# Performance work log

Measured on AMD Instinct MI355X. Metric: run time of the kernel, lower is better.

## Reference

```python
import jax, jax.numpy as jnp
import numpy as np

B, S, D, H = 4, 2048, 1024, 16
DK = D // H


def setup_inputs() -> dict:
    key = jax.random.key(0)
    kx, kq, kk, kv, ko = jax.random.split(key, 5)
    scale = D ** -0.5
    return {
        "x": jax.random.normal(kx, (B, S, D), dtype=jnp.float32),
        "W_q": jax.random.normal(kq, (D, D), dtype=jnp.float32) * scale,
        "W_k": jax.random.normal(kk, (D, D), dtype=jnp.float32) * scale,
        "W_v": jax.random.normal(kv, (D, D), dtype=jnp.float32) * scale,
        "W_o": jax.random.normal(ko, (D, D), dtype=jnp.float32) * scale,
    }


def reference(x, W_q, W_k, W_v, W_o):
    b, s, d = x.shape
    # projections: x @ W.T  (weights stored [out, in])
    def proj(W):
        return (x @ W.T).reshape(b, s, H, DK).transpose(0, 2, 1, 3)  # [b,h,s,dk]
    Q, K, V = proj(W_q), proj(W_k), proj(W_v)
    scores = jnp.einsum('bhqd,bhkd->bhqk', Q, K) * (DK ** -0.5)
    causal = jnp.tril(jnp.ones((s, s), dtype=bool))
    scores = jnp.where(causal, scores, -jnp.inf)
    attn = jax.nn.softmax(scores, axis=-1)
    out = jnp.einsum('bhqk,bhkd->bhqd', attn, V)  # [b,h,s,dk]
    out = out.transpose(0, 2, 1, 3).reshape(b, s, d)
    return out @ W_o.T
```

## Files before the change

kernel.cpp:

```cpp
#include <hip/hip_runtime.h>
#include <stdint.h>

#define B_ 4
#define S_ 2048
#define D_ 1024
#define H_ 16
#define DK_ 64
#define M_ (B_*S_)

typedef __attribute__((ext_vector_type(8))) short bhalf8;
typedef __attribute__((ext_vector_type(4))) short bhalf4;
typedef __attribute__((ext_vector_type(4))) float floatx4;
typedef unsigned short bfu;
typedef unsigned int u32;

__device__ __forceinline__ bfu f2bf(float f) {
  union { float f; u32 u; } v; v.f = f;
  u32 r = v.u + 0x7FFFu + ((v.u >> 16) & 1u);
  return (bfu)(r >> 16);
}

__device__ __forceinline__ u32 cvtpk(float a, float b) {
  u32 r;
  asm("v_cvt_pk_bf16_f32 %0, %1, %2" : "=v"(r) : "v"(a), "v"(b));
  return r;
}

__device__ __forceinline__ void gll16(const bfu* g, bfu* l) {
  __builtin_amdgcn_global_load_lds((__attribute__((address_space(1))) void*)g,
                                   (__attribute__((address_space(3))) void*)l,
                                   16, 0, 0);
}

__global__ void cvt_all(const float* __restrict__ x,  const float* __restrict__ wq,
                        const float* __restrict__ wk, const float* __restrict__ wv,
                        const float* __restrict__ wo, bfu* __restrict__ dst) {
  const size_t u = ((size_t)blockIdx.x * blockDim.x + threadIdx.x) * 4;
  const size_t XN = (size_t)M_ * D_;
  const float* src;
  if (u < XN) {
    src = x + u;
  } else {
    const size_t v = u - XN;
    const int wsel = (int)(v >> 20);
    const size_t off = v & ((size_t)(1u << 20) - 1);
    src = ((wsel == 0) ? wq : (wsel == 1) ? wk : (wsel == 2) ? wv : wo) + off;
  }
  float4 vv = *(const float4*)src;
  ushort4 o;
  o.x = f2bf(vv.x); o.y = f2bf(vv.y); o.z = f2bf(vv.z); o.w = f2bf(vv.w);
  *(ushort4*)(dst + u) = o;
}

__device__ __forceinline__ void gemm_core_2ph(const bfu* __restrict__ A,
                                              const bfu* __restrict__ Bw,
                                              bfu* smem,
                                              int m0, int bn0,
                                              floatx4 (&acc)[4][4])
{
  const int tid  = threadIdx.x;
  const int lane = tid & 63;
  const int g    = lane >> 4;
  const int i16  = lane & 15;
  const int w    = tid >> 6;
  const int wm   = w >> 1, wn = w & 1;

  const int lrow = lane >> 3;
  const int scol = ((lane & 7) ^ lrow) << 3;
  const bfu* As = A  + (size_t)(m0  + w * 32 + lrow) * D_ + scol;
  const bfu* Bs = Bw + (size_t)(bn0 + w * 32 + lrow) * D_ + scol;
  const int ldst = w * 4 * 512;

  auto STAGE = [&](int t) {
    bfu* base = smem + (t & 1) * 16384;
    const int k0 = t * 64;
#pragma unroll
    for (int j = 0; j < 4; ++j)
      gll16(As + (size_t)j * 8 * D_ + k0, base + ldst + j * 512);
#pragma unroll
    for (int j = 0; j < 4; ++j)
      gll16(Bs + (size_t)j * 8 * D_ + k0, base + 8192 + ldst + j * 512);
  };

  auto COMPUTE = [&](int t) {
    const char* aTc = (const char*)(smem + (t & 1) * 16384);
    const char* bTc = aTc + 16384;
    __builtin_amdgcn_s_setprio(1);
#pragma unroll
    for (int kb = 0; kb < 2; ++kb) {
      bhalf8 af[4], bf[4];
#pragma unroll
      for (int f = 0; f < 4; ++f) {
        int arow = wm * 64 + f * 16 + i16;
        af[f] = *(const bhalf8*)(aTc + arow * 128 + ((kb * 64 + g * 16) ^ ((arow & 7) << 4)));
        int brow = wn * 64 + f * 16 + i16;
        bf[f] = *(const bhalf8*)(bTc + brow * 128 + ((kb * 64 + g * 16) ^ ((brow & 7) << 4)));
      }
#pragma unroll
      for (int fm = 0; fm < 4; ++fm)
#pragma unroll
        for (int fn = 0; fn < 4; ++fn)
          acc[fm][fn] = __builtin_amdgcn_mfma_f32_16x16x32_bf16(af[fm], bf[fn], acc[fm][fn], 0, 0, 0);
    }
    __builtin_amdgcn_s_setprio(0);
  };

  STAGE(0);
  __syncthreads();
  for (int t = 0; t < 16; ++t) {
    if (t + 1 < 16) STAGE(t + 1);
    COMPUTE(t);
    __syncthreads();
  }
}

__global__ __launch_bounds__(256) void qkv_gemm(const bfu* __restrict__ xb,
                                                const bfu* __restrict__ wqkv,
                                                bfu* __restrict__ Qd,
                                                bfu* __restrict__ Kd,
                                                bfu* __restrict__ Vtd)
{
  __shared__ bfu smem[2 * 16384];
  const int bid = blockIdx.x;
  const int wi   = bid >> 3;
  const int xblk = wi >> 3;
  const int y    = ((bid & 7) << 3) | (wi & 7);
  const int m0   = y * 128;
  const int z    = xblk >> 3;
  const int n0   = (xblk & 7) * 128;
  const int bn0  = xblk * 128;

  floatx4 acc[4][4] = {};
  gemm_core_2ph(xb, wqkv, smem, m0, bn0, acc);

  bfu* dst = (z == 0) ? Qd : (z == 1) ? Kd : Vtd;
  const int lane = threadIdx.x & 63;
  const int g = lane >> 4, i16 = lane & 15;
  const int w = threadIdx.x >> 6, wm = w >> 1, wn = w & 1;
#pragma unroll
  for (int fm = 0; fm < 4; ++fm) {
#pragma unroll
    for (int fn = 0; fn < 4; ++fn) {
      int col = n0 + wn * 64 + fn * 16 + i16;
      int h = col >> 6, dk = col & 63;
#pragma unroll
      for (int r = 0; r < 4; ++r) {
        int mrow = m0 + wm * 64 + fm * 16 + g * 4 + r;
        int b = mrow >> 11, s = mrow & (S_ - 1);
        size_t idx = (z == 2)
            ? ((size_t)((b * H_ + h) * DK_ + dk)) * S_ + s
            : ((size_t)((b * H_ + h) * S_ + s)) * DK_ + dk;
        dst[idx] = f2bf(acc[fm][fn][r]);
      }
    }
  }
}

__global__ __launch_bounds__(256) void out_gemm(const bfu* __restrict__ Ab,
                                                const bfu* __restrict__ wob,
                                                float* __restrict__ out)
{
  __shared__ bfu smem[2 * 16384];
  const int bid = blockIdx.x;
  const int wi   = bid >> 3;
  const int xblk = wi >> 3;
  const int y    = ((bid & 7) << 3) | (wi & 7);
  const int m0   = y * 128;
  const int n0   = xblk * 128;

  floatx4 acc[4][4] = {};
  gemm_core_2ph(Ab, wob, smem, m0, n0, acc);

  const int lane = threadIdx.x & 63;
  const int g = lane >> 4, i16 = lane & 15;
  const int w = threadIdx.x >> 6, wm = w >> 1, wn = w & 1;
#pragma unroll
  for (int fm = 0; fm < 4; ++fm)
#pragma unroll
    for (int fn = 0; fn < 4; ++fn) {
      int col = n0 + wn * 64 + fn * 16 + i16;
#pragma unroll
      for (int r = 0; r < 4; ++r) {
        int mrow = m0 + wm * 64 + fm * 16 + g * 4 + r;
        out[(size_t)mrow * D_ + col] = acc[fm][fn][r];
      }
    }
}

template<int BUF>
__device__ __forceinline__ void attn_tile(const char* smem, int t, int ntw, int qr,
                                          int koff0, int koff1, const int (&voff)[4],
                                          bhalf8 qa0, bhalf8 qa1, int g, int i16,
                                          floatx4 (&ot)[4], float& mC2, float& lp)
{
  const float C2 = 0.125f * 1.44269504f;
  floatx4 sa[4] = {};
#pragma unroll
  for (int cb = 0; cb < 4; ++cb) {
    bhalf8 kf0 = *(const bhalf8*)(smem + BUF + cb * 2048 + koff0);
    bhalf8 kf1 = *(const bhalf8*)(smem + BUF + cb * 2048 + koff1);
    sa[cb] = __builtin_amdgcn_mfma_f32_16x16x32_bf16(kf0, qa0, sa[cb], 0, 0, 0);
    sa[cb] = __builtin_amdgcn_mfma_f32_16x16x32_bf16(kf1, qa1, sa[cb], 0, 0, 0);
  }
  if (t == ntw - 1) {
    const int kv0 = t * 64;
#pragma unroll
    for (int cb = 0; cb < 4; ++cb)
#pragma unroll
      for (int r = 0; r < 4; ++r)
        if (kv0 + cb * 16 + g * 4 + r > qr + i16) sa[cb][r] = -3.0e38f;
  }
  float pm = sa[0][0];
#pragma unroll
  for (int cb = 0; cb < 4; ++cb)
#pragma unroll
    for (int r = 0; r < 4; ++r)
      pm = fmaxf(pm, sa[cb][r]);
  pm = fmaxf(pm, __shfl_xor(pm, 16));
  pm = fmaxf(pm, __shfl_xor(pm, 32));
  const float pmC2 = pm * C2;
  if (!__all(pmC2 - mC2 <= 8.0f)) {
    const float nmax = fmaxf(mC2, pmC2);
    const float al = exp2f(mC2 - nmax);
    mC2 = nmax;
    lp *= al;
#pragma unroll
    for (int da = 0; da < 4; ++da)
#pragma unroll
      for (int r = 0; r < 4; ++r)
        ot[da][r] *= al;
  }
  const float nm = -mC2;
  u32 pk[8];
  float ps = 0.f;
#pragma unroll
  for (int cb = 0; cb < 4; ++cb) {
    float p0 = exp2f(__builtin_fmaf(sa[cb][0], C2, nm));
    float p1 = exp2f(__builtin_fmaf(sa[cb][1], C2, nm));
    float p2 = exp2f(__builtin_fmaf(sa[cb][2], C2, nm));
    float p3 = exp2f(__builtin_fmaf(sa[cb][3], C2, nm));
    ps += (p0 + p1) + (p2 + p3);
    pk[cb * 2]     = cvtpk(p0, p1);
    pk[cb * 2 + 1] = cvtpk(p2, p3);
  }
  lp += ps;
#pragma unroll
  for (int da = 0; da < 4; ++da) {
#pragma unroll
    for (int cb = 0; cb < 4; ++cb) {
      bhalf4 vf = *(const bhalf4*)(smem + BUF + voff[cb] + da * 2048);
      union { u32 u[2]; bhalf4 h; } pu;
      pu.u[0] = pk[cb * 2]; pu.u[1] = pk[cb * 2 + 1];
      ot[da] = __builtin_amdgcn_mfma_f32_16x16x16bf16_1k(vf, pu.h, ot[da], 0, 0, 0);
    }
  }
}

__global__ __launch_bounds__(512, 4) void attn_kernel(const bfu* __restrict__ Q,
                                                      const bfu* __restrict__ Kc,
                                                      const bfu* __restrict__ Vt,
                                                      bfu* __restrict__ Oc)
{
  __shared__ char smem[2 * 16384];
  const int tid = threadIdx.x;
  const int lane = tid & 63;
  const int w = tid >> 6;
  const int g = lane >> 4, i16 = lane & 15;
  const int sw = (i16 & 7) << 4;
  const int bh = blockIdx.x;
  const int y0 = blockIdx.y;

  const bfu* Qb = Q  + (size_t)bh * S_ * DK_;
  const bfu* Kb = Kc + (size_t)bh * S_ * DK_;
  const bfu* Vb = Vt + (size_t)bh * DK_ * S_;
  const int b = bh >> 4, h = bh & 15;

  const int srow = tid >> 3;
  const int scolb = (tid & 7) * 16;
  const bfu* kgp = Kb + srow * DK_ + (scolb >> 1);
  const bfu* vgp = Vb + (size_t)srow * S_ + (scolb >> 1);
  char* kld = smem + srow * 128 + (scolb ^ ((srow & 7) << 4));
  const int vsw = ((srow & 7) << 4) | (srow & 8);
  char* vld0 = smem + 8192 + srow * 128 + ((scolb    ) ^ vsw);
  char* vld1 = smem + 8192 + srow * 128 + ((scolb + 8) ^ vsw);

  const int koff0 = i16 * 128 + ((g * 16) ^ sw);
  const int koff1 = i16 * 128 + ((64 + g * 16) ^ sw);
  const int vswr = sw | (i16 & 8);
  int voff[4];
#pragma unroll
  for (int cb = 0; cb < 4; ++cb)
    voff[cb] = 8192 + i16 * 128 + ((cb * 32 + g * 8) ^ vswr);

  for (int pass = 0; pass < 2; ++pass) {
    const int y = pass ? (15 - y0) : y0;
    const int ntw = 2 * y + 1 + (w >> 2);
    const int qr = y * 128 + w * 16;
    const int spine = 2 * y + 2;

    bhalf8 qa0 = *(const bhalf8*)(Qb + (size_t)(qr + i16) * DK_ + g * 8);
    bhalf8 qa1 = *(const bhalf8*)(Qb + (size_t)(qr + i16) * DK_ + 32 + g * 8);

    floatx4 ot[4] = {};
    float mC2 = -1.0e30f;
    float lp  = 0.f;

    union { bhalf8 h8; bhalf4 h4[2]; } vu;
    bhalf8 kst = *(const bhalf8*)kgp;
    bhalf8 vst = *(const bhalf8*)vgp;
    *(bhalf8*)kld = kst;
    vu.h8 = vst;
    *(bhalf4*)vld0 = vu.h4[0]; *(bhalf4*)vld1 = vu.h4[1];
    __syncthreads();

    const int half = spine >> 1;
    for (int i = 0; ; ++i) {
      const int t0 = 2 * i, t1 = 2 * i + 1;
      const bool more = (i + 1 < half);
      kst = *(const bhalf8*)(kgp + (size_t)t1 * 4096);
      vst = *(const bhalf8*)(vgp + t1 * 64);
      if (t0 < ntw)
        attn_tile<0>(smem, t0, ntw, qr, koff0, koff1, voff, qa0, qa1, g, i16, ot, mC2, lp);
      *(bhalf8*)(kld + 16384) = kst;
      vu.h8 = vst;
      *(bhalf4*)(vld0 + 16384) = vu.h4[0]; *(bhalf4*)(vld1 + 16384) = vu.h4[1];
      __syncthreads();
      if (more) {
        kst = *(const bhalf8*)(kgp + (size_t)(t0 + 2) * 4096);
        vst = *(const bhalf8*)(vgp + (t0 + 2) * 64);
      }
      if (t1 < ntw)
        attn_tile<16384>(smem, t1, ntw, qr, koff0, koff1, voff, qa0, qa1, g, i16, ot, mC2, lp);
      if (!more) break;
      *(bhalf8*)kld = kst;
      vu.h8 = vst;
      *(bhalf4*)vld0 = vu.h4[0]; *(bhalf4*)vld1 = vu.h4[1];
      __syncthreads();
    }
    __syncthreads();

    float lt = lp;
    lt += __shfl_xor(lt, 16);
    lt += __shfl_xor(lt, 32);
    const float rl = 1.0f / lt;
    const size_t rowbase = (size_t)(b * S_ + qr + i16) * D_ + h * 64;
#pragma unroll
    for (int da = 0; da < 4; ++da) {
      union { u32 u[2]; uint2 v; } ov;
      ov.u[0] = cvtpk(ot[da][0] * rl, ot[da][1] * rl);
      ov.u[1] = cvtpk(ot[da][2] * rl, ot[da][3] * rl);
      *(uint2*)(Oc + rowbase + da * 16 + g * 4) = ov.v;
    }
  }
}

extern "C" void kernel_launch(void* const* d_in, const int* in_sizes, int n_in,
                              void* d_out, int out_size, void* d_ws, size_t ws_size,
                              hipStream_t stream)
{
  const float* x  = (const float*)d_in[0];
  const float* wq = (const float*)d_in[1];
  const float* wk = (const float*)d_in[2];
  const float* wv = (const float*)d_in[3];
  const float* wo = (const float*)d_in[4];

  bfu* xb  = (bfu*)d_ws;
  bfu* wqb = xb  + (size_t)M_ * D_;
  bfu* wob = wqb + (size_t)3 * D_ * D_;
  bfu* Qd  = wob + (size_t)D_ * D_;
  bfu* Kd  = Qd  + (size_t)M_ * D_;
  bfu* Vtd = Kd  + (size_t)M_ * D_;
  bfu* Ad  = Vtd + (size_t)M_ * D_;

  const size_t total = (size_t)M_ * D_ + 4 * (size_t)D_ * D_;
  cvt_all<<<(int)(total / 4 / 256), 256, 0, stream>>>(x, wq, wk, wv, wo, xb);

  qkv_gemm<<<1536, 256, 0, stream>>>(xb, wqb, Qd, Kd, Vtd);
  attn_kernel<<<dim3(B_ * H_, 8), 512, 0, stream>>>(Qd, Kd, Vtd, Ad);
  out_gemm<<<512, 256, 0, stream>>>(Ad, wob, (float*)d_out);
}
```

Baseline: 183.4 us.

## Stage K/V tiles in pairs with a double-buffered 64KB LDS pipeline

Restructures the attention K/V staging so each pipeline step loads two 64-key tiles into shared memory. It double-buffers these pairs across four LDS slots, which halves the number of __syncthreads barriers per key tile and gives the global loads more time to complete. The cost is doubled shared memory (64KB per block), which may cut the number of resident blocks below the launch_bounds target of 4, and more registers for the staged loads.

After: 184.4 us. Within noise of the previous version (+0.6%).

```diff
diff --git a/kernel.cpp b/kernel.cpp
--- a/kernel.cpp
+++ b/kernel.cpp
@@ -261,7 +261,7 @@
                                                       const bfu* __restrict__ Vt,
                                                       bfu* __restrict__ Oc)
 {
-  __shared__ char smem[2 * 16384];
+  __shared__ char smem[2 * 32768];
   const int tid = threadIdx.x;
   const int lane = tid & 63;
   const int w = tid >> 6;
@@ -296,7 +296,7 @@
     const int y = pass ? (15 - y0) : y0;
     const int ntw = 2 * y + 1 + (w >> 2);
     const int qr = y * 128 + w * 16;
-    const int spine = 2 * y + 2;
+    const int npair = y + 1;
 
     bhalf8 qa0 = *(const bhalf8*)(Qb + (size_t)(qr + i16) * DK_ + g * 8);
     bhalf8 qa1 = *(const bhalf8*)(Qb + (size_t)(qr + i16) * DK_ + 32 + g * 8);
@@ -306,35 +306,55 @@
     float lp  = 0.f;
 
     union { bhalf8 h8; bhalf4 h4[2]; } vu;
-    bhalf8 kst = *(const bhalf8*)kgp;
-    bhalf8 vst = *(const bhalf8*)vgp;
-    *(bhalf8*)kld = kst;
-    vu.h8 = vst;
-    *(bhalf4*)vld0 = vu.h4[0]; *(bhalf4*)vld1 = vu.h4[1];
+    bhalf8 ka, va, kb2, vb2;
+    ka  = *(const bhalf8*)kgp;                  va  = *(const bhalf8*)vgp;
+    kb2 = *(const bhalf8*)(kgp + 4096);         vb2 = *(const bhalf8*)(vgp + 64);
+    *(bhalf8*)kld = ka;  vu.h8 = va;  *(bhalf4*)vld0 = vu.h4[0]; *(bhalf4*)vld1 = vu.h4[1];
+    *(bhalf8*)(kld + 16384) = kb2; vu.h8 = vb2;
+    *(bhalf4*)(vld0 + 16384) = vu.h4[0]; *(bhalf4*)(vld1 + 16384) = vu.h4[1];
     __syncthreads();
 
-    const int half = spine >> 1;
     for (int i = 0; ; ++i) {
-      const int t0 = 2 * i, t1 = 2 * i + 1;
-      const bool more = (i + 1 < half);
-      kst = *(const bhalf8*)(kgp + (size_t)t1 * 4096);
-      vst = *(const bhalf8*)(vgp + t1 * 64);
-      if (t0 < ntw)
+      const int pa = 2 * i + 1;
+      const bool morea = (pa < npair);
+      if (morea) {
+        ka  = *(const bhalf8*)(kgp + (size_t)(2 * pa)     * 4096);
+        va  = *(const bhalf8*)(vgp + (2 * pa)     * 64);
+        kb2 = *(const bhalf8*)(kgp + (size_t)(2 * pa + 1) * 4096);
+        vb2 = *(const bhalf8*)(vgp + (2 * pa + 1) * 64);
+      }
+      {
+        const int t0 = 4 * i;
         attn_tile<0>(smem, t0, ntw, qr, koff0, koff1, voff, qa0, qa1, g, i16, ot, mC2, lp);
-      *(bhalf8*)(kld + 16384) = kst;
-      vu.h8 = vst;
+        if (t0 + 1 < ntw)
+          attn_tile<16384>(smem, t0 + 1, ntw, qr, koff0, koff1, voff, qa0, qa1, g, i16, ot, mC2, lp);
+      }
+      if (!morea) break;
+      *(bhalf8*)(kld + 32768) = ka;  vu.h8 = va;
+      *(bhalf4*)(vld0 + 32768) = vu.h4[0]; *(bhalf4*)(vld1 + 32768) = vu.h4[1];
+      *(bhalf8*)(kld + 49152) = kb2; vu.h8 = vb2;
+      *(bhalf4*)(vld0 + 49152) = vu.h4[0]; *(bhalf4*)(vld1 + 49152) = vu.h4[1];
+      __syncthreads();
+
+      const int pb = 2 * i + 2;
+      const bool moreb = (pb < npair);
+      if (moreb) {
+        ka  = *(const bhalf8*)(kgp + (size_t)(2 * pb)     * 4096);
+        va  = *(const bhalf8*)(vgp + (2 * pb)     * 64);
+        kb2 = *(const bhalf8*)(kgp + (size_t)(2 * pb + 1) * 4096);
+        vb2 = *(const bhalf8*)(vgp + (2 * pb + 1) * 64);
+      }
+      {
+        const int t0 = 4 * i + 2;
+        attn_tile<32768>(smem, t0, ntw, qr, koff0, koff1, voff, qa0, qa1, g, i16, ot, mC2, lp);
+        if (t0 + 1 < ntw)
+          attn_tile<49152>(smem, t0 + 1, ntw, qr, koff0, koff1, voff, qa0, qa1, g, i16, ot, mC2, lp);
+      }
+      if (!moreb) break;
+      *(bhalf8*)kld = ka;  vu.h8 = va;
+      *(bhalf4*)vld0 = vu.h4[0]; *(bhalf4*)vld1 = vu.h4[1];
+      *(bhalf8*)(kld + 16384) = kb2; vu.h8 = vb2;
       *(bhalf4*)(vld0 + 16384) = vu.h4[0]; *(bhalf4*)(vld1 + 16384) = vu.h4[1];
-      __syncthreads();
-      if (more) {
-        kst = *(const bhalf8*)(kgp + (size_t)(t0 + 2) * 4096);
-        vst = *(const bhalf8*)(vgp + (t0 + 2) * 64);
-      }
-      if (t1 < ntw)
-        attn_tile<16384>(smem, t1, ntw, qr, koff0, koff1, voff, qa0, qa1, g, i16, ot, mC2, lp);
-      if (!more) break;
-      *(bhalf8*)kld = kst;
-      vu.h8 = vst;
-      *(bhalf4*)vld0 = vu.h4[0]; *(bhalf4*)vld1 = vu.h4[1];
       __syncthreads();
     }
     __syncthreads();
```

## Split attention into one query block per workgroup, heaviest first, with paired K/V staging

Applied to the files above, without the earlier changes.

Each attention workgroup previously handled two complementary causal query blocks (y and 15-y) to balance work. Now it handles a single query block, the grid doubles to 16 blocks per head, and blocks are ordered longest-first so the hardware scheduler balances the load. The K/V pipeline now loads two tiles per iteration and stages both buffers between barriers, and the launch bound asks for 8 workgroups per CU. The goal is more parallelism and occupancy, at the cost of losing the explicit pairing balance, leaving less of the global loads hidden behind compute, and adding register pressure.

Measured after the change: 266.0 us. +45.0%, slower.

```diff
diff --git a/kernel.cpp b/kernel.cpp
--- a/kernel.cpp
+++ b/kernel.cpp
@@ -256,19 +256,19 @@
   }
 }
 
-__global__ __launch_bounds__(512, 4) void attn_kernel(const bfu* __restrict__ Q,
+__global__ __launch_bounds__(512, 8) void attn_kernel(const bfu* __restrict__ Q,
                                                       const bfu* __restrict__ Kc,
                                                       const bfu* __restrict__ Vt,
                                                       bfu* __restrict__ Oc)
 {
-  __shared__ char smem[2 * 16384];
+  __shared__ char smem[32768];
   const int tid = threadIdx.x;
   const int lane = tid & 63;
   const int w = tid >> 6;
   const int g = lane >> 4, i16 = lane & 15;
   const int sw = (i16 & 7) << 4;
   const int bh = blockIdx.x;
-  const int y0 = blockIdx.y;
+  const int y  = 15 - blockIdx.y;
 
   const bfu* Qb = Q  + (size_t)bh * S_ * DK_;
   const bfu* Kb = Kc + (size_t)bh * S_ * DK_;
@@ -292,65 +292,58 @@
   for (int cb = 0; cb < 4; ++cb)
     voff[cb] = 8192 + i16 * 128 + ((cb * 32 + g * 8) ^ vswr);
 
-  for (int pass = 0; pass < 2; ++pass) {
-    const int y = pass ? (15 - y0) : y0;
-    const int ntw = 2 * y + 1 + (w >> 2);
-    const int qr = y * 128 + w * 16;
-    const int spine = 2 * y + 2;
-
-    bhalf8 qa0 = *(const bhalf8*)(Qb + (size_t)(qr + i16) * DK_ + g * 8);
-    bhalf8 qa1 = *(const bhalf8*)(Qb + (size_t)(qr + i16) * DK_ + 32 + g * 8);
-
-    floatx4 ot[4] = {};
-    float mC2 = -1.0e30f;
-    float lp  = 0.f;
-
-    union { bhalf8 h8; bhalf4 h4[2]; } vu;
-    bhalf8 kst = *(const bhalf8*)kgp;
-    bhalf8 vst = *(const bhalf8*)vgp;
-    *(bhalf8*)kld = kst;
-    vu.h8 = vst;
+  const int ntw = 2 * y + 1 + (w >> 2);
+  const int qr = y * 128 + w * 16;
+  const int npair = y + 1;
+
+  bhalf8 qa0 = *(const bhalf8*)(Qb + (size_t)(qr + i16) * DK_ + g * 8);
+  bhalf8 qa1 = *(const bhalf8*)(Qb + (size_t)(qr + i16) * DK_ + 32 + g * 8);
+
+  floatx4 ot[4] = {};
+  float mC2 = -1.0e30f;
+  float lp  = 0.f;
+
+  union { bhalf8 h8; bhalf4 h4[2]; } vu;
+  bhalf8 ka, va, kb2, vb2;
+  ka  = *(const bhalf8*)kgp;                  va  = *(const bhalf8*)vgp;
+  kb2 = *(const bhalf8*)(kgp + 4096);         vb2 = *(const bhalf8*)(vgp + 64);
+  *(bhalf8*)kld = ka;  vu.h8 = va;  *(bhalf4*)vld0 = vu.h4[0]; *(bhalf4*)vld1 = vu.h4[1];
+  *(bhalf8*)(kld + 16384) = kb2; vu.h8 = vb2;
+  *(bhalf4*)(vld0 + 16384) = vu.h4[0]; *(bhalf4*)(vld1 + 16384) = vu.h4[1];
+  __syncthreads();
+
+  for (int p = 0; ; ++p) {
+    const bool more = (p + 1 < npair);
+    if (more) {
+      ka  = *(const bhalf8*)(kgp + (size_t)(2 * p + 2) * 4096);
+      va  = *(const bhalf8*)(vgp + (2 * p + 2) * 64);
+      kb2 = *(const bhalf8*)(kgp + (size_t)(2 * p + 3) * 4096);
+      vb2 = *(const bhalf8*)(vgp + (2 * p + 3) * 64);
+    }
+    const int t0 = 2 * p;
+    attn_tile<0>(smem, t0, ntw, qr, koff0, koff1, voff, qa0, qa1, g, i16, ot, mC2, lp);
+    if (t0 + 1 < ntw)
+      attn_tile<16384>(smem, t0 + 1, ntw, qr, koff0, koff1, voff, qa0, qa1, g, i16, ot, mC2, lp);
+    if (!more) break;
+    __syncthreads();
+    *(bhalf8*)kld = ka;  vu.h8 = va;
     *(bhalf4*)vld0 = vu.h4[0]; *(bhalf4*)vld1 = vu.h4[1];
+    *(bhalf8*)(kld + 16384) = kb2; vu.h8 = vb2;
+    *(bhalf4*)(vld0 + 16384) = vu.h4[0]; *(bhalf4*)(vld1 + 16384) = vu.h4[1];
     __syncthreads();
-
-    const int half = spine >> 1;
-    for (int i = 0; ; ++i) {
-      const int t0 = 2 * i, t1 = 2 * i + 1;
-      const bool more = (i + 1 < half);
-      kst = *(const bhalf8*)(kgp + (size_t)t1 * 4096);
-      vst = *(const bhalf8*)(vgp + t1 * 64);
-      if (t0 < ntw)
-        attn_tile<0>(smem, t0, ntw, qr, koff0, koff1, voff, qa0, qa1, g, i16, ot, mC2, lp);
-      *(bhalf8*)(kld + 16384) = kst;
-      vu.h8 = vst;
-      *(bhalf4*)(vld0 + 16384) = vu.h4[0]; *(bhalf4*)(vld1 + 16384) = vu.h4[1];
-      __syncthreads();
-      if (more) {
-        kst = *(const bhalf8*)(kgp + (size_t)(t0 + 2) * 4096);
-        vst = *(const bhalf8*)(vgp + (t0 + 2) * 64);
-      }
-      if (t1 < ntw)
-        attn_tile<16384>(smem, t1, ntw, qr, koff0, koff1, voff, qa0, qa1, g, i16, ot, mC2, lp);
-      if (!more) break;
-      *(bhalf8*)kld = kst;
-      vu.h8 = vst;
-      *(bhalf4*)vld0 = vu.h4[0]; *(bhalf4*)vld1 = vu.h4[1];
-      __syncthreads();
-    }
-    __syncthreads();
-
-    float lt = lp;
-    lt += __shfl_xor(lt, 16);
-    lt += __shfl_xor(lt, 32);
-    const float rl = 1.0f / lt;
-    const size_t rowbase = (size_t)(b * S_ + qr + i16) * D_ + h * 64;
-#pragma unroll
-    for (int da = 0; da < 4; ++da) {
-      union { u32 u[2]; uint2 v; } ov;
-      ov.u[0] = cvtpk(ot[da][0] * rl, ot[da][1] * rl);
-      ov.u[1] = cvtpk(ot[da][2] * rl, ot[da][3] * rl);
-      *(uint2*)(Oc + rowbase + da * 16 + g * 4) = ov.v;
-    }
+  }
+
+  float lt = lp;
+  lt += __shfl_xor(lt, 16);
+  lt += __shfl_xor(lt, 32);
+  const float rl = 1.0f / lt;
+  const size_t rowbase = (size_t)(b * S_ + qr + i16) * D_ + h * 64;
+#pragma unroll
+  for (int da = 0; da < 4; ++da) {
+    union { u32 u[2]; uint2 v; } ov;
+    ov.u[0] = cvtpk(ot[da][0] * rl, ot[da][1] * rl);
+    ov.u[1] = cvtpk(ot[da][2] * rl, ot[da][3] * rl);
+    *(uint2*)(Oc + rowbase + da * 16 + g * 4) = ov.v;
   }
 }
 
@@ -376,6 +369,6 @@
   cvt_all<<<(int)(total / 4 / 256), 256, 0, stream>>>(x, wq, wk, wv, wo, xb);
 
   qkv_gemm<<<1536, 256, 0, stream>>>(xb, wqb, Qd, Kd, Vtd);
-  attn_kernel<<<dim3(B_ * H_, 8), 512, 0, stream>>>(Qd, Kd, Vtd, Ad);
+  attn_kernel<<<dim3(B_ * H_, 16), 512, 0, stream>>>(Qd, Kd, Vtd, Ad);
   out_gemm<<<512, 256, 0, stream>>>(Ad, wob, (float*)d_out);
 }
```
